# Optimization experiments

Measured on AMD Instinct MI355X. Metric: run time of the kernel, lower is better.

Reference implementation:

```python
import jax, jax.numpy as jnp
import numpy as np

N = 200000          # real (non-pad) faces
P = 8192            # pad entries
PAD = N + P         # padded table size
C_IN = 128
C_OUT = 128


def setup_inputs() -> dict:
    key = jax.random.key(0)
    ks = jax.random.split(key, 6)
    x = jax.random.normal(ks[0], (N, C_IN), jnp.float32)
    # column 0 = the face itself (a real, non-pad index); columns 1..8 = neighbors
    col0 = jnp.arange(N, dtype=jnp.int64)[:, None]
    nbrs = jax.random.randint(ks[1], (N, 8), 0, PAD, dtype=jnp.int64)
    face_neighborhood = jnp.concatenate([col0, nbrs], axis=1)
    face_is_pad = jnp.arange(PAD) >= N  # last P rows are padding
    s = 1.0 / np.sqrt(C_IN).astype(np.float32)
    in_proj_w = jax.random.normal(ks[2], (3 * C_IN, C_IN), jnp.float32) * s
    in_proj_b = jnp.zeros((3 * C_IN,), jnp.float32)
    out_proj_w = jax.random.normal(ks[3], (C_IN, C_IN), jnp.float32) * s
    out_proj_b = jnp.zeros((C_IN,), jnp.float32)
    conv_w = jax.random.normal(ks[4], (C_OUT, C_IN, 1, 2), jnp.float32) * (1.0 / np.sqrt(2.0 * C_IN).astype(np.float32))
    conv_b = jnp.zeros((C_OUT,), jnp.float32)
    return {
        "x": x,
        "face_neighborhood": face_neighborhood,
        "face_is_pad": face_is_pad,
        "pad_size": PAD,
        "in_proj_w": in_proj_w,
        "in_proj_b": in_proj_b,
        "out_proj_w": out_proj_w,
        "out_proj_b": out_proj_b,
        "conv_w": conv_w,
        "conv_b": conv_b,
    }


def reference(x, face_neighborhood, face_is_pad, pad_size,
              in_proj_w, in_proj_b, out_proj_w, out_proj_b, conv_w, conv_b):
    C = x.shape[1]
    H = max(1, C // 32)
    Dh = C // H
    # scatter real features into the padded table (padded_x[~face_is_pad] = x)
    nonpad_idx = jnp.nonzero(~face_is_pad, size=x.shape[0])[0]
    padded_x = jnp.zeros((pad_size, C), x.dtype).at[nonpad_idx].set(x)
    f = padded_x[face_neighborhood]              # [N, 9, C] 9-way gather
    center = f[:, 0]                             # [N, C] query feature
    kv = f[:, 1:]                                # [N, 8, C]
    # torch MultiheadAttention: packed in_proj then per-head scaled dot-product
    q = (center @ in_proj_w[:C].T + in_proj_b[:C]).reshape(-1, 1, H, Dh).transpose(0, 2, 1, 3)       # [N,H,1,Dh]
    k = (kv @ in_proj_w[C:2 * C].T + in_proj_b[C:2 * C]).reshape(-1, 8, H, Dh).transpose(0, 2, 1, 3)  # [N,H,8,Dh]
    v = (kv @ in_proj_w[2 * C:].T + in_proj_b[2 * C:]).reshape(-1, 8, H, Dh).transpose(0, 2, 1, 3)    # [N,H,8,Dh]
    scale = 1.0 / jnp.sqrt(jnp.asarray(Dh, q.dtype))
    scores = jnp.einsum('nhqd,nhkd->nhqk', q, k) * scale  # [N,H,1,8]
    pad_mask = face_is_pad[face_neighborhood[:, 1:]][:, None, None, :]  # [N,1,1,8]
    scores = jnp.where(pad_mask, -jnp.inf, scores)
    attn = jax.nn.softmax(scores, axis=-1)
    o = jnp.einsum('nhqk,nhkd->nhqd', attn, v)            # [N,H,1,Dh]
    o = o.transpose(0, 2, 1, 3).reshape(-1, C)            # [N,C] (q_len==1)
    h = o @ out_proj_w.T + out_proj_b                     # [N,C]
    # Conv2d(C_in, C_out, (1,2)) over [N, C, 1, 2] == linear fuse of center & h
    out = center @ conv_w[:, :, 0, 0].T + h @ conv_w[:, :, 0, 1].T + conv_b  # [N, C_out]
    return out
```

## Files before the change

### kernel.cpp

```cpp
#include <hip/hip_runtime.h>

typedef __bf16 bfrag __attribute__((ext_vector_type(8)));
typedef float f32x4 __attribute__((ext_vector_type(4)));

__device__ __forceinline__ unsigned short f2bf(float f) {
  unsigned u = __float_as_uint(f);
  u = (u + 0x7fffu + ((u >> 16) & 1u)) >> 16;
  return (unsigned short)u;
}
__device__ __forceinline__ float bflo(unsigned u) {
  return __uint_as_float(u << 16);
}
__device__ __forceinline__ float bfhi(unsigned u) {
  return __uint_as_float(u & 0xffff0000u);
}

#define LDB 72
#define LDE 76
#define LDO 36

__global__ void k_prep(const float* __restrict__ in_proj_w,
                       const float* __restrict__ conv_w,
                       const float* __restrict__ out_proj_w,
                       const float* __restrict__ out_proj_b,
                       const float* __restrict__ conv_b,
                       unsigned short* __restrict__ Wcat,
                       unsigned short* __restrict__ W2cat,
                       float* __restrict__ cvec) {
  int b = blockIdx.x, t = threadIdx.x;
  if (b < 384) {
    Wcat[b * 128 + t] = f2bf(in_proj_w[b * 128 + t]);
  } else {
    int c = b - 384;
    float s = 0.f;
    for (int k = 0; k < 128; ++k)
      s += conv_w[(c * 128 + k) * 2 + 1] * out_proj_w[k * 128 + t];
    W2cat[c * 256 + t] = f2bf(s);
    W2cat[c * 256 + 128 + t] = f2bf(conv_w[(c * 128 + t) * 2]);
    if (t == 0) {
      float cs = conv_b[c];
      for (int k = 0; k < 128; ++k)
        cs += conv_w[(c * 128 + k) * 2 + 1] * out_proj_b[k];
      cvec[c] = cs;
    }
  }
}

__global__ __launch_bounds__(256) void k_gemm_qkv(
    const float* __restrict__ x, const unsigned short* __restrict__ Wcat,
    const float* __restrict__ in_proj_b, unsigned short* __restrict__ Qb,
    unsigned short* __restrict__ KVb, int M) {
  __shared__ unsigned short sb[128 * LDB];
  __shared__ unsigned short se[128 * LDE];
  const int m0 = blockIdx.x * 128;
  const int t = threadIdx.x;
  const int w = t >> 6, lane = t & 63, quad = lane >> 4, mr = lane & 15;

  bfrag af[4][2];
#pragma unroll
  for (int ks = 0; ks < 4; ++ks)
#pragma unroll
    for (int r = 0; r < 2; ++r) {
      int row = m0 + w * 32 + r * 16 + mr;
      union { unsigned short s[8]; bfrag f; } u;
      if (row < M) {
        const float4* p =
            reinterpret_cast<const float4*>(&x[(size_t)row * 128 + ks * 32 + quad * 8]);
        float4 v0 = p[0], v1 = p[1];
        u.s[0] = f2bf(v0.x); u.s[1] = f2bf(v0.y); u.s[2] = f2bf(v0.z); u.s[3] = f2bf(v0.w);
        u.s[4] = f2bf(v1.x); u.s[5] = f2bf(v1.y); u.s[6] = f2bf(v1.z); u.s[7] = f2bf(v1.w);
      } else {
#pragma unroll
        for (int i = 0; i < 8; ++i) u.s[i] = 0;
      }
      af[ks][r] = u.f;
    }

#pragma unroll
  for (int cb = 0; cb < 3; ++cb) {
    f32x4 acc[2][8];
#pragma unroll
    for (int r = 0; r < 2; ++r)
#pragma unroll
      for (int c = 0; c < 8; ++c) acc[r][c] = (f32x4){0.f, 0.f, 0.f, 0.f};

#pragma unroll
    for (int kh = 0; kh < 2; ++kh) {
      __syncthreads();
#pragma unroll
      for (int i = 0; i < 4; ++i) {
        int ch = t + 256 * i;
        int row = ch >> 3, col8 = ch & 7;
        uint4 v = *reinterpret_cast<const uint4*>(
            &Wcat[(size_t)(cb * 128 + row) * 128 + kh * 64 + col8 * 8]);
        *reinterpret_cast<uint4*>(&sb[row * LDB + col8 * 8]) = v;
      }
      __syncthreads();
#pragma unroll
      for (int ks2 = 0; ks2 < 2; ++ks2) {
        int ks = kh * 2 + ks2;
        int k0 = ks2 * 32 + quad * 8;
#pragma unroll
        for (int c = 0; c < 8; ++c) {
          bfrag b = *reinterpret_cast<const bfrag*>(&sb[(c * 16 + mr) * LDB + k0]);
          acc[0][c] = __builtin_amdgcn_mfma_f32_16x16x32_bf16(af[ks][0], b, acc[0][c], 0, 0, 0);
          acc[1][c] = __builtin_amdgcn_mfma_f32_16x16x32_bf16(af[ks][1], b, acc[1][c], 0, 0, 0);
        }
      }
    }
    const float* bias = in_proj_b + cb * 128;
    unsigned short* dst = (cb == 0) ? Qb : KVb;
    const int ldst = (cb == 0) ? 128 : 256;
    const int cb_off = (cb == 2) ? 128 : 0;
#pragma unroll
    for (int p = 0; p < 2; ++p) {
      __syncthreads();
#pragma unroll
      for (int r = 0; r < 2; ++r)
#pragma unroll
        for (int cc = 0; cc < 4; ++cc) {
          int c = p * 4 + cc;
          float bv = bias[c * 16 + mr];
#pragma unroll
          for (int g = 0; g < 4; ++g) {
            int row = w * 32 + r * 16 + quad * 4 + g;
            se[row * LDE + cc * 16 + mr] = f2bf(acc[r][c][g] + bv);
          }
        }
      __syncthreads();
#pragma unroll
      for (int i = 0; i < 4; ++i) {
        int ch = t + 256 * i;
        int row = ch >> 3, col8 = ch & 7;
        if (m0 + row < M) {
          uint2 lo = *reinterpret_cast<const uint2*>(&se[row * LDE + col8 * 8]);
          uint2 hi = *reinterpret_cast<const uint2*>(&se[row * LDE + col8 * 8 + 4]);
          uint4 v = {lo.x, lo.y, hi.x, hi.y};
          *reinterpret_cast<uint4*>(
              &dst[(size_t)(m0 + row) * ldst + cb_off + p * 64 + col8 * 8]) = v;
        }
      }
    }
  }
}

__global__ __launch_bounds__(256) void k_attn(
    const unsigned short* __restrict__ Qb, const unsigned short* __restrict__ KVb,
    const int* __restrict__ fn, unsigned short* __restrict__ Ob, int M) {
  int w = threadIdx.x >> 6, lane = threadIdx.x & 63;
  int n = blockIdx.x * 4 + w;
  if (n >= M) return;
  const float scale = 0.17677669529663687f;
  const int l5 = lane & 31;
  uint2 qp = *reinterpret_cast<const uint2*>(&Qb[(size_t)n * 128 + 4 * l5]);
  float q0 = bflo(qp.x), q1 = bfhi(qp.x), q2 = bflo(qp.y), q3 = bfhi(qp.y);
  int idx[8];
#pragma unroll
  for (int j = 0; j < 8; ++j) idx[j] = fn[n * 9 + 1 + j];
  float o0 = 0.f, o1 = 0.f, o2 = 0.f, o3 = 0.f, sum = 0.f;
#pragma unroll
  for (int j = 0; j < 8; ++j) {
    bool valid = idx[j] < M;
    int id = valid ? idx[j] : 0;
    uint2 kv = *reinterpret_cast<const uint2*>(&KVb[(size_t)id * 256 + 4 * lane]);
    float a0 = bflo(kv.x), a1 = bfhi(kv.x), a2 = bflo(kv.y), a3 = bfhi(kv.y);
    float p = q0 * a0 + q1 * a1 + q2 * a2 + q3 * a3;
    p += __shfl_xor(p, 1);
    p += __shfl_xor(p, 2);
    p += __shfl_xor(p, 4);
    float pu = __shfl_xor(p, 32);
    float sf = (lane >= 32) ? pu : p;
    float s = valid ? sf * scale : -1e30f;
    float e = __expf(s);
    sum += e;
    o0 += e * a0; o1 += e * a1; o2 += e * a2; o3 += e * a3;
  }
  float inv = 1.f / sum;
  if (lane >= 32) {
    union { unsigned short s[4]; uint2 u; } p;
    p.s[0] = f2bf(o0 * inv); p.s[1] = f2bf(o1 * inv);
    p.s[2] = f2bf(o2 * inv); p.s[3] = f2bf(o3 * inv);
    *reinterpret_cast<uint2*>(&Ob[(size_t)n * 128 + 4 * l5]) = p.u;
  }
}

__global__ __launch_bounds__(256) void k_gemm_out(
    const unsigned short* __restrict__ Ob, const float* __restrict__ x,
    const unsigned short* __restrict__ W2cat, const float* __restrict__ cvec,
    float* __restrict__ out, int M) {
  __shared__ unsigned short sb[128 * LDB];
  __shared__ float sf[128 * LDO];
  const int m0 = blockIdx.x * 128;
  const int t = threadIdx.x;
  const int w = t >> 6, lane = t & 63, quad = lane >> 4, mr = lane & 15;

  f32x4 acc[2][8];
#pragma unroll
  for (int r = 0; r < 2; ++r)
#pragma unroll
    for (int c = 0; c < 8; ++c) acc[r][c] = (f32x4){0.f, 0.f, 0.f, 0.f};

#pragma unroll
  for (int kc = 0; kc < 4; ++kc) {
    bfrag af[2][2];
#pragma unroll
    for (int ks2 = 0; ks2 < 2; ++ks2)
#pragma unroll
      for (int r = 0; r < 2; ++r) {
        int row = m0 + w * 32 + r * 16 + mr;
        if (kc < 2) {
          union { uint4 v; bfrag f; } u;
          u.v = make_uint4(0u, 0u, 0u, 0u);
          if (row < M)
            u.v = *reinterpret_cast<const uint4*>(
                &Ob[(size_t)row * 128 + kc * 64 + ks2 * 32 + quad * 8]);
          af[ks2][r] = u.f;
        } else {
          union { unsigned short s[8]; bfrag f; } u;
          if (row < M) {
            const float4* p = reinterpret_cast<const float4*>(
                &x[(size_t)row * 128 + (kc - 2) * 64 + ks2 * 32 + quad * 8]);
            float4 v0 = p[0], v1 = p[1];
            u.s[0] = f2bf(v0.x); u.s[1] = f2bf(v0.y); u.s[2] = f2bf(v0.z); u.s[3] = f2bf(v0.w);
            u.s[4] = f2bf(v1.x); u.s[5] = f2bf(v1.y); u.s[6] = f2bf(v1.z); u.s[7] = f2bf(v1.w);
          } else {
#pragma unroll
            for (int i = 0; i < 8; ++i) u.s[i] = 0;
          }
          af[ks2][r] = u.f;
        }
      }
    __syncthreads();
#pragma unroll
    for (int i = 0; i < 4; ++i) {
      int ch = t + 256 * i;
      int row = ch >> 3, col8 = ch & 7;
      uint4 v = *reinterpret_cast<const uint4*>(&W2cat[(size_t)row * 256 + kc * 64 + col8 * 8]);
      *reinterpret_cast<uint4*>(&sb[row * LDB + col8 * 8]) = v;
    }
    __syncthreads();
#pragma unroll
    for (int ks2 = 0; ks2 < 2; ++ks2) {
      int k0 = ks2 * 32 + quad * 8;
#pragma unroll
      for (int c = 0; c < 8; ++c) {
        bfrag b = *reinterpret_cast<const bfrag*>(&sb[(c * 16 + mr) * LDB + k0]);
        acc[0][c] = __builtin_amdgcn_mfma_f32_16x16x32_bf16(af[ks2][0], b, acc[0][c], 0, 0, 0);
        acc[1][c] = __builtin_amdgcn_mfma_f32_16x16x32_bf16(af[ks2][1], b, acc[1][c], 0, 0, 0);
      }
    }
  }
#pragma unroll
  for (int p = 0; p < 4; ++p) {
    __syncthreads();
#pragma unroll
    for (int r = 0; r < 2; ++r)
#pragma unroll
      for (int cc = 0; cc < 2; ++cc) {
        int c = p * 2 + cc;
        float cv = cvec[c * 16 + mr];
#pragma unroll
        for (int g = 0; g < 4; ++g) {
          int row = w * 32 + r * 16 + quad * 4 + g;
          sf[row * LDO + cc * 16 + mr] = acc[r][c][g] + cv;
        }
      }
    __syncthreads();
#pragma unroll
    for (int i = 0; i < 4; ++i) {
      int ch = t + 256 * i;
      int row = ch >> 3, col4 = ch & 7;
      if (m0 + row < M) {
        float4 v = *reinterpret_cast<const float4*>(&sf[row * LDO + col4 * 4]);
        *reinterpret_cast<float4*>(&out[(size_t)(m0 + row) * 128 + p * 32 + col4 * 4]) = v;
      }
    }
  }
}

extern "C" void kernel_launch(void* const* d_in, const int* in_sizes, int n_in,
                              void* d_out, int out_size, void* d_ws, size_t ws_size,
                              hipStream_t stream) {
  const float* x          = (const float*)d_in[0];
  const int*   fn         = (const int*)d_in[1];
  const float* in_proj_w  = (const float*)d_in[4];
  const float* in_proj_b  = (const float*)d_in[5];
  const float* out_proj_w = (const float*)d_in[6];
  const float* out_proj_b = (const float*)d_in[7];
  const float* conv_w     = (const float*)d_in[8];
  const float* conv_b     = (const float*)d_in[9];
  const int M = in_sizes[0] / 128;

  unsigned short* KVb = (unsigned short*)d_out;
  char* ws = (char*)d_ws;
  unsigned short* Qb    = (unsigned short*)ws;
  unsigned short* Ob    = (unsigned short*)(ws + (size_t)M * 128 * 2);
  unsigned short* Wcat  = (unsigned short*)(ws + (size_t)M * 128 * 4);
  unsigned short* W2cat = Wcat + 384 * 128;
  float*          cvec  = (float*)(W2cat + 128 * 256);

  const int mt = (M + 127) / 128;
  k_prep<<<dim3(512), dim3(128), 0, stream>>>(in_proj_w, conv_w, out_proj_w,
                                              out_proj_b, conv_b, Wcat, W2cat, cvec);
  k_gemm_qkv<<<dim3(mt), dim3(256), 0, stream>>>(x, Wcat, in_proj_b, Qb, KVb, M);
  k_attn<<<dim3((M + 3) / 4), dim3(256), 0, stream>>>(Qb, KVb, fn, Ob, M);
  k_gemm_out<<<dim3(mt), dim3(256), 0, stream>>>(Ob, x, W2cat, cvec, (float*)d_out, M);
}
```

Baseline: 455.5 us.

## Pre-swizzle weights into MFMA fragment layout and drop LDS staging barriers

```diff
diff --git a/kernel.cpp b/kernel.cpp
--- a/kernel.cpp
+++ b/kernel.cpp
@@ -8,35 +8,40 @@
   u = (u + 0x7fffu + ((u >> 16) & 1u)) >> 16;
   return (unsigned short)u;
 }
-__device__ __forceinline__ float bflo(unsigned u) {
-  return __uint_as_float(u << 16);
-}
-__device__ __forceinline__ float bfhi(unsigned u) {
-  return __uint_as_float(u & 0xffff0000u);
-}
-
-#define LDB 72
-#define LDE 76
-#define LDO 36
+__device__ __forceinline__ float bflo(unsigned u) { return __uint_as_float(u << 16); }
+__device__ __forceinline__ float bfhi(unsigned u) { return __uint_as_float(u & 0xffff0000u); }
 
 __global__ void k_prep(const float* __restrict__ in_proj_w,
                        const float* __restrict__ conv_w,
                        const float* __restrict__ out_proj_w,
                        const float* __restrict__ out_proj_b,
                        const float* __restrict__ conv_b,
-                       unsigned short* __restrict__ Wcat,
-                       unsigned short* __restrict__ W2cat,
+                       unsigned short* __restrict__ WcatF,
+                       unsigned short* __restrict__ W2F,
                        float* __restrict__ cvec) {
   int b = blockIdx.x, t = threadIdx.x;
   if (b < 384) {
-    Wcat[b * 128 + t] = f2bf(in_proj_w[b * 128 + t]);
+    unsigned short v = f2bf(in_proj_w[b * 128 + t]);
+    int cb = b >> 7, r7 = b & 127;
+    int cB = r7 >> 4, mr = r7 & 15;
+    int ks = t >> 5, quad = (t >> 3) & 3, j = t & 7;
+    WcatF[(((cb * 8 + cB) * 4 + ks) << 9) + (quad * 16 + mr) * 8 + j] = v;
   } else {
     int c = b - 384;
+    int cB = c >> 4, mr = c & 15;
     float s = 0.f;
     for (int k = 0; k < 128; ++k)
       s += conv_w[(c * 128 + k) * 2 + 1] * out_proj_w[k * 128 + t];
-    W2cat[c * 256 + t] = f2bf(s);
-    W2cat[c * 256 + 128 + t] = f2bf(conv_w[(c * 128 + t) * 2]);
+    {
+      int kc = t >> 6, ks2 = (t >> 5) & 1, quad = (t >> 3) & 3, j = t & 7;
+      W2F[(((cB * 4 + kc) * 2 + ks2) << 9) + (quad * 16 + mr) * 8 + j] = f2bf(s);
+    }
+    {
+      int K = 128 + t;
+      int kc = K >> 6, ks2 = (K >> 5) & 1, quad = (K >> 3) & 3, j = K & 7;
+      W2F[(((cB * 4 + kc) * 2 + ks2) << 9) + (quad * 16 + mr) * 8 + j] =
+          f2bf(conv_w[(c * 128 + t) * 2]);
+    }
     if (t == 0) {
       float cs = conv_b[c];
       for (int k = 0; k < 128; ++k)
@@ -46,15 +51,15 @@
   }
 }
 
-__global__ __launch_bounds__(256) void k_gemm_qkv(
-    const float* __restrict__ x, const unsigned short* __restrict__ Wcat,
+__global__ __launch_bounds__(256, 4) void k_gemm_qkv(
+    const float* __restrict__ x, const unsigned short* __restrict__ WcatF,
     const float* __restrict__ in_proj_b, unsigned short* __restrict__ Qb,
     unsigned short* __restrict__ KVb, int M) {
-  __shared__ unsigned short sb[128 * LDB];
-  __shared__ unsigned short se[128 * LDE];
+  __shared__ unsigned short se[4][32 * 72];
   const int m0 = blockIdx.x * 128;
   const int t = threadIdx.x;
   const int w = t >> 6, lane = t & 63, quad = lane >> 4, mr = lane & 15;
+  unsigned short* sew = se[w];
 
   bfrag af[4][2];
 #pragma unroll
@@ -78,66 +83,45 @@
 
 #pragma unroll
   for (int cb = 0; cb < 3; ++cb) {
-    f32x4 acc[2][8];
-#pragma unroll
-    for (int r = 0; r < 2; ++r)
-#pragma unroll
-      for (int c = 0; c < 8; ++c) acc[r][c] = (f32x4){0.f, 0.f, 0.f, 0.f};
-
-#pragma unroll
-    for (int kh = 0; kh < 2; ++kh) {
-      __syncthreads();
-#pragma unroll
-      for (int i = 0; i < 4; ++i) {
-        int ch = t + 256 * i;
-        int row = ch >> 3, col8 = ch & 7;
-        uint4 v = *reinterpret_cast<const uint4*>(
-            &Wcat[(size_t)(cb * 128 + row) * 128 + kh * 64 + col8 * 8]);
-        *reinterpret_cast<uint4*>(&sb[row * LDB + col8 * 8]) = v;
-      }
-      __syncthreads();
-#pragma unroll
-      for (int ks2 = 0; ks2 < 2; ++ks2) {
-        int ks = kh * 2 + ks2;
-        int k0 = ks2 * 32 + quad * 8;
-#pragma unroll
-        for (int c = 0; c < 8; ++c) {
-          bfrag b = *reinterpret_cast<const bfrag*>(&sb[(c * 16 + mr) * LDB + k0]);
-          acc[0][c] = __builtin_amdgcn_mfma_f32_16x16x32_bf16(af[ks][0], b, acc[0][c], 0, 0, 0);
-          acc[1][c] = __builtin_amdgcn_mfma_f32_16x16x32_bf16(af[ks][1], b, acc[1][c], 0, 0, 0);
-        }
-      }
-    }
-    const float* bias = in_proj_b + cb * 128;
     unsigned short* dst = (cb == 0) ? Qb : KVb;
     const int ldst = (cb == 0) ? 128 : 256;
     const int cb_off = (cb == 2) ? 128 : 0;
 #pragma unroll
-    for (int p = 0; p < 2; ++p) {
-      __syncthreads();
+    for (int half = 0; half < 2; ++half) {
+      f32x4 acc[2][4];
 #pragma unroll
       for (int r = 0; r < 2; ++r)
 #pragma unroll
-        for (int cc = 0; cc < 4; ++cc) {
-          int c = p * 4 + cc;
+        for (int c = 0; c < 4; ++c) acc[r][c] = (f32x4){0.f, 0.f, 0.f, 0.f};
+#pragma unroll
+      for (int ks = 0; ks < 4; ++ks)
+#pragma unroll
+        for (int c = 0; c < 4; ++c) {
+          union { uint4 v; bfrag f; } u;
+          u.v = *reinterpret_cast<const uint4*>(
+              &WcatF[(((cb * 8 + half * 4 + c) * 4 + ks) << 9) + lane * 8]);
+          acc[0][c] = __builtin_amdgcn_mfma_f32_16x16x32_bf16(af[ks][0], u.f, acc[0][c], 0, 0, 0);
+          acc[1][c] = __builtin_amdgcn_mfma_f32_16x16x32_bf16(af[ks][1], u.f, acc[1][c], 0, 0, 0);
+        }
+      const float* bias = in_proj_b + cb * 128 + half * 64;
+#pragma unroll
+      for (int r = 0; r < 2; ++r)
+#pragma unroll
+        for (int c = 0; c < 4; ++c) {
           float bv = bias[c * 16 + mr];
 #pragma unroll
-          for (int g = 0; g < 4; ++g) {
-            int row = w * 32 + r * 16 + quad * 4 + g;
-            se[row * LDE + cc * 16 + mr] = f2bf(acc[r][c][g] + bv);
-          }
-        }
-      __syncthreads();
+          for (int g = 0; g < 4; ++g)
+            sew[(r * 16 + quad * 4 + g) * 72 + c * 16 + mr] = f2bf(acc[r][c][g] + bv);
+        }
 #pragma unroll
       for (int i = 0; i < 4; ++i) {
-        int ch = t + 256 * i;
-        int row = ch >> 3, col8 = ch & 7;
-        if (m0 + row < M) {
-          uint2 lo = *reinterpret_cast<const uint2*>(&se[row * LDE + col8 * 8]);
-          uint2 hi = *reinterpret_cast<const uint2*>(&se[row * LDE + col8 * 8 + 4]);
-          uint4 v = {lo.x, lo.y, hi.x, hi.y};
+        int ch = i * 64 + lane;
+        int row = ch >> 3, cp = ch & 7;
+        int grow = m0 + w * 32 + row;
+        if (grow < M) {
+          uint4 v = *reinterpret_cast<const uint4*>(&sew[row * 72 + cp * 8]);
           *reinterpret_cast<uint4*>(
-              &dst[(size_t)(m0 + row) * ldst + cb_off + p * 64 + col8 * 8]) = v;
+              &dst[(size_t)grow * ldst + cb_off + half * 64 + cp * 8]) = v;
         }
       }
     }
@@ -184,15 +168,15 @@
   }
 }
 
-__global__ __launch_bounds__(256) void k_gemm_out(
+__global__ __launch_bounds__(256, 4) void k_gemm_out(
     const unsigned short* __restrict__ Ob, const float* __restrict__ x,
-    const unsigned short* __restrict__ W2cat, const float* __restrict__ cvec,
+    const unsigned short* __restrict__ W2F, const float* __restrict__ cvec,
     float* __restrict__ out, int M) {
-  __shared__ unsigned short sb[128 * LDB];
-  __shared__ float sf[128 * LDO];
+  __shared__ float sf[4][32 * 36];
   const int m0 = blockIdx.x * 128;
   const int t = threadIdx.x;
   const int w = t >> 6, lane = t & 63, quad = lane >> 4, mr = lane & 15;
+  float* sfw = sf[w];
 
   f32x4 acc[2][8];
 #pragma unroll
@@ -230,49 +214,37 @@
           af[ks2][r] = u.f;
         }
       }
-    __syncthreads();
+#pragma unroll
+    for (int ks2 = 0; ks2 < 2; ++ks2)
+#pragma unroll
+      for (int c = 0; c < 8; ++c) {
+        union { uint4 v; bfrag f; } u;
+        u.v = *reinterpret_cast<const uint4*>(
+            &W2F[(((c * 4 + kc) * 2 + ks2) << 9) + lane * 8]);
+        acc[0][c] = __builtin_amdgcn_mfma_f32_16x16x32_bf16(af[ks2][0], u.f, acc[0][c], 0, 0, 0);
+        acc[1][c] = __builtin_amdgcn_mfma_f32_16x16x32_bf16(af[ks2][1], u.f, acc[1][c], 0, 0, 0);
+      }
+  }
+#pragma unroll
+  for (int p = 0; p < 4; ++p) {
+#pragma unroll
+    for (int cc = 0; cc < 2; ++cc) {
+      int c = p * 2 + cc;
+      float cv = cvec[c * 16 + mr];
+#pragma unroll
+      for (int r = 0; r < 2; ++r)
+#pragma unroll
+        for (int g = 0; g < 4; ++g)
+          sfw[(r * 16 + quad * 4 + g) * 36 + cc * 16 + mr] = acc[r][c][g] + cv;
+    }
 #pragma unroll
     for (int i = 0; i < 4; ++i) {
-      int ch = t + 256 * i;
-      int row = ch >> 3, col8 = ch & 7;
-      uint4 v = *reinterpret_cast<const uint4*>(&W2cat[(size_t)row * 256 + kc * 64 + col8 * 8]);
-      *reinterpret_cast<uint4*>(&sb[row * LDB + col8 * 8]) = v;
-    }
-    __syncthreads();
-#pragma unroll
-    for (int ks2 = 0; ks2 < 2; ++ks2) {
-      int k0 = ks2 * 32 + quad * 8;
-#pragma unroll
-      for (int c = 0; c < 8; ++c) {
-        bfrag b = *reinterpret_cast<const bfrag*>(&sb[(c * 16 + mr) * LDB + k0]);
-        acc[0][c] = __builtin_amdgcn_mfma_f32_16x16x32_bf16(af[ks2][0], b, acc[0][c], 0, 0, 0);
-        acc[1][c] = __builtin_amdgcn_mfma_f32_16x16x32_bf16(af[ks2][1], b, acc[1][c], 0, 0, 0);
-      }
-    }
-  }
-#pragma unroll
-  for (int p = 0; p < 4; ++p) {
-    __syncthreads();
-#pragma unroll
-    for (int r = 0; r < 2; ++r)
-#pragma unroll
-      for (int cc = 0; cc < 2; ++cc) {
-        int c = p * 2 + cc;
-        float cv = cvec[c * 16 + mr];
-#pragma unroll
-        for (int g = 0; g < 4; ++g) {
-          int row = w * 32 + r * 16 + quad * 4 + g;
-          sf[row * LDO + cc * 16 + mr] = acc[r][c][g] + cv;
-        }
-      }
-    __syncthreads();
-#pragma unroll
-    for (int i = 0; i < 4; ++i) {
-      int ch = t + 256 * i;
-      int row = ch >> 3, col4 = ch & 7;
-      if (m0 + row < M) {
-        float4 v = *reinterpret_cast<const float4*>(&sf[row * LDO + col4 * 4]);
-        *reinterpret_cast<float4*>(&out[(size_t)(m0 + row) * 128 + p * 32 + col4 * 4]) = v;
+      int ch = i * 64 + lane;
+      int row = ch >> 3, c4 = ch & 7;
+      int grow = m0 + w * 32 + row;
+      if (grow < M) {
+        float4 v = *reinterpret_cast<const float4*>(&sfw[row * 36 + c4 * 4]);
+        *reinterpret_cast<float4*>(&out[(size_t)grow * 128 + p * 32 + c4 * 4]) = v;
       }
     }
   }
@@ -295,14 +267,14 @@
   char* ws = (char*)d_ws;
   unsigned short* Qb    = (unsigned short*)ws;
   unsigned short* Ob    = (unsigned short*)(ws + (size_t)M * 128 * 2);
-  unsigned short* Wcat  = (unsigned short*)(ws + (size_t)M * 128 * 4);
-  unsigned short* W2cat = Wcat + 384 * 128;
-  float*          cvec  = (float*)(W2cat + 128 * 256);
+  unsigned short* WcatF = (unsigned short*)(ws + (size_t)M * 128 * 4);
+  unsigned short* W2F   = WcatF + 384 * 128;
+  float*          cvec  = (float*)(W2F + 128 * 256);
 
   const int mt = (M + 127) / 128;
   k_prep<<<dim3(512), dim3(128), 0, stream>>>(in_proj_w, conv_w, out_proj_w,
-                                              out_proj_b, conv_b, Wcat, W2cat, cvec);
-  k_gemm_qkv<<<dim3(mt), dim3(256), 0, stream>>>(x, Wcat, in_proj_b, Qb, KVb, M);
+                                              out_proj_b, conv_b, WcatF, W2F, cvec);
+  k_gemm_qkv<<<dim3(mt), dim3(256), 0, stream>>>(x, WcatF, in_proj_b, Qb, KVb, M);
   k_attn<<<dim3((M + 3) / 4), dim3(256), 0, stream>>>(Qb, KVb, fn, Ob, M);
-  k_gemm_out<<<dim3(mt), dim3(256), 0, stream>>>(Ob, x, W2cat, cvec, (float*)d_out, M);
-}
+  k_gemm_out<<<dim3(mt), dim3(256), 0, stream>>>(Ob, x, W2F, cvec, (float*)d_out, M);
+}
```

Measured after the change: 441.1 us. 3.2% less time.
